# Optimization experiments

Hardware: AMD Instinct MI355X
Metric: run time of the kernel (lower is better)

## Reference

```python
import jax, jax.numpy as jnp
import numpy as np

VOCAB = 4194304
EMBED = 128
BATCH = 16384
NUM_DENSE = 13
NUM_CAT = 26
BOT_DIMS = (512, 256, 128)
TOP_DIMS = (1024, 1024, 512, 256, 1)


def _dense_params(key, fan_in, fan_out):
    kw, kb = jax.random.split(key)
    w = jax.random.normal(kw, (fan_in, fan_out), jnp.float32) * np.sqrt(2.0 / (fan_in + fan_out))
    b = jax.random.normal(kb, (fan_out,), jnp.float32) * np.sqrt(1.0 / fan_out)
    return w, b


def setup_inputs() -> dict:
    key = jax.random.key(0)
    ks = jax.random.split(key, 16)
    inp = {}
    inp['x_dense'] = jax.random.normal(ks[0], (BATCH, NUM_DENSE), jnp.float32)
    inp['x_cat'] = jax.random.randint(ks[1], (BATCH, NUM_CAT), 0, VOCAB, dtype=jnp.int32)
    # embedding table: uniform(0,1) * 1/sqrt(vocab)
    inp['embedding_table'] = jax.random.uniform(ks[2], (VOCAB, EMBED), jnp.float32) * np.float32(1.0 / np.sqrt(VOCAB))
    # bottom MLP params
    fan_in = NUM_DENSE
    for i, d in enumerate(BOT_DIMS):
        w, b = _dense_params(ks[3 + i], fan_in, d)
        inp[f'w_bot{i}'], inp[f'b_bot{i}'] = w, b
        fan_in = d
    # top MLP params; input dim = embed_dim + n_triu(27) = 128 + 378 = 506
    n_feat = 1 + NUM_CAT  # 27
    fan_in = EMBED + n_feat * (n_feat + 1) // 2
    for i, d in enumerate(TOP_DIMS):
        w, b = _dense_params(ks[8 + i], fan_in, d)
        inp[f'w_top{i}'], inp[f'b_top{i}'] = w, b
        fan_in = d
    return inp


def _forward(x_dense, x_cat, embedding_table,
             w_bot0, b_bot0, w_bot1, b_bot1, w_bot2, b_bot2,
             w_top0, b_top0, w_top1, b_top1, w_top2, b_top2,
             w_top3, b_top3, w_top4, b_top4):
    B = x_dense.shape[0]
    # bottom MLP
    h = x_dense
    for w, b in ((w_bot0, b_bot0), (w_bot1, b_bot1), (w_bot2, b_bot2)):
        h = jax.nn.relu(h @ w + b)
    bot_out = h  # [B, 128]
    feat = bot_out.reshape(B, -1, EMBED)  # [B, 1, 128]
    # embedding gather (irregular access)
    idx = (x_cat.reshape(-1) % VOCAB)
    emb = embedding_table[idx].reshape(B, NUM_CAT, EMBED)  # [B, 26, 128]
    stack = jnp.concatenate([feat, emb], axis=1)  # [B, 27, 128]
    # self interaction + upper-triangular (incl. diagonal) extraction
    xact = jnp.einsum('bnd,bmd->bnm', stack, stack)  # [B, 27, 27]
    i, j = jnp.triu_indices(stack.shape[1])
    inter = xact[:, i, j]  # [B, 378]
    top = jnp.concatenate([bot_out, inter], axis=-1)  # [B, 506]
    tops = ((w_top0, b_top0), (w_top1, b_top1), (w_top2, b_top2), (w_top3, b_top3), (w_top4, b_top4))
    for li, (w, b) in enumerate(tops):
        top = top @ w + b
        if li < len(tops) - 1:
            top = jax.nn.relu(top)
    return top  # [B, 1] logits


def reference(x_dense, x_cat, embedding_table,
              w_bot0, b_bot0, w_bot1, b_bot1, w_bot2, b_bot2,
              w_top0, b_top0, w_top1, b_top1, w_top2, b_top2,
              w_top3, b_top3, w_top4, b_top4):
    return _forward(x_dense, x_cat, embedding_table,
                    w_bot0, b_bot0, w_bot1, b_bot1, w_bot2, b_bot2,
                    w_top0, b_top0, w_top1, b_top1, w_top2, b_top2,
                    w_top3, b_top3, w_top4, b_top4)
```

## Files before the change

### kernel.cpp

```cpp
#include <hip/hip_runtime.h>
#include <cstdint>
#include <cstddef>

#define BATCH 16384
#define VOCAB_MASK (4194304 - 1)

typedef __attribute__((ext_vector_type(4))) float f32x4;
typedef __attribute__((ext_vector_type(8))) __bf16 bf16x8;

static_assert(sizeof(bf16x8) == 16, "bf16x8 must be 16 bytes");

static __device__ __forceinline__ __bf16 f2bf(float f) {
  union { float f; unsigned u; } in; in.f = f;
  unsigned r = in.u + 0x7FFF + ((in.u >> 16) & 1);
  union { unsigned short s; __bf16 b; } out; out.s = (unsigned short)(r >> 16);
  return out.b;
}
static __device__ __forceinline__ float bf2f(__bf16 b) {
  union { __bf16 b; unsigned short s; } in; in.b = b;
  union { unsigned u; float f; } out; out.u = ((unsigned)in.s) << 16;
  return out.f;
}

#define GLDS16(g, l) __builtin_amdgcn_global_load_lds( \
    (const __attribute__((address_space(1))) unsigned int*)(g), \
    (__attribute__((address_space(3))) unsigned int*)(l), 16, 0, 0)

static __device__ __forceinline__ unsigned swz16(unsigned b) {
  return b ^ ((((b >> 6) & 3u) ^ ((b >> 8) & 3u)) << 4);
}
static __device__ __forceinline__ bf16x8 lds_frag(const char* smem, unsigned base,
                                                  unsigned r, unsigned cg) {
  unsigned b = r * 64u + cg;
  return *(const bf16x8*)(smem + base + swz16(b));
}

struct TJob { const float* W; __bf16* WT; int K, N, Kp, tx, off; };
struct TJobs { TJob j[7]; };

__global__ __launch_bounds__(256) void transpose_all(TJobs js, int njobs)
{
  __shared__ float tile[64][65];
  int b = blockIdx.x;
  int ji = 0;
  #pragma unroll
  for (int i = 1; i < 7; ++i) if (i < njobs && b >= js.j[i].off) ji = i;
  const TJob jb = js.j[ji];
  int lb = b - jb.off;
  int bx = lb % jb.tx, by = lb / jb.tx;
  const int kb = bx * 64, nb = by * 64;
  const int tx = threadIdx.x & 63, ty = threadIdx.x >> 6;
  #pragma unroll
  for (int i = 0; i < 64; i += 4) {
    int k = kb + ty + i, n = nb + tx;
    tile[ty + i][tx] = (k < jb.K && n < jb.N) ? jb.W[(size_t)k * jb.N + n] : 0.f;
  }
  __syncthreads();
  #pragma unroll
  for (int i = 0; i < 64; i += 4) {
    int n = nb + ty + i, k = kb + tx;
    if (n < jb.N && k < jb.Kp) jb.WT[(size_t)n * jb.Kp + k] = f2bf(tile[tx][ty + i]);
  }
}

__global__ __launch_bounds__(256) void bottom_fused(
    const float* __restrict__ x,
    const __bf16* __restrict__ w0t, const float* __restrict__ b0,
    const __bf16* __restrict__ w1t, const float* __restrict__ b1,
    const __bf16* __restrict__ w2t, const float* __restrict__ b2,
    __bf16* __restrict__ h2out)
{
  __shared__ __bf16 h0s[32][520];
  __shared__ __bf16 h1s[32][264];
  __shared__ __bf16 As[32][40];
  __shared__ __bf16 Bs[256][32];
  const int tid = threadIdx.x, lane = tid & 63, w = tid >> 6;
  const int r0 = blockIdx.x * 32;
  const int srow_b = lane >> 2;
  const int scol_b = (lane & 3) * 8;
  const unsigned rA = lane & 15, cgw = (lane >> 4) * 8;

  for (int idx = tid; idx < 32 * 40; idx += 256) {
    int row = idx / 40, k = idx - row * 40;
    float v = (k < 13) ? x[(size_t)(r0 + row) * 13 + k] : 0.f;
    As[row][k] = f2bf(v);
  }

  #pragma unroll
  for (int p = 0; p < 2; ++p) {
    __syncthreads();
    #pragma unroll
    for (int c = 0; c < 4; ++c) {
      int row = w * 64 + c * 16 + srow_b;
      GLDS16(w0t + (size_t)(p * 256 + row) * 32 + scol_b, &Bs[row][scol_b]);
    }
    __syncthreads();
    bf16x8 a[2], bv[4];
    #pragma unroll
    for (int m = 0; m < 2; ++m) a[m] = *(const bf16x8*)&As[rA + m * 16][cgw];
    #pragma unroll
    for (int n = 0; n < 4; ++n) bv[n] = *(const bf16x8*)&Bs[w * 64 + n * 16 + rA][cgw];
    f32x4 acc[2][4] = {};
    #pragma unroll
    for (int m = 0; m < 2; ++m)
      #pragma unroll
      for (int n = 0; n < 4; ++n)
        acc[m][n] = __builtin_amdgcn_mfma_f32_16x16x32_bf16(a[m], bv[n], acc[m][n], 0, 0, 0);
    #pragma unroll
    for (int m = 0; m < 2; ++m)
      #pragma unroll
      for (int n = 0; n < 4; ++n) {
        int col = p * 256 + w * 64 + n * 16 + (int)rA;
        float bb = b0[col];
        #pragma unroll
        for (int r = 0; r < 4; ++r) {
          int row = m * 16 + (lane >> 4) * 4 + r;
          h0s[row][col] = f2bf(fmaxf(acc[m][n][r] + bb, 0.f));
        }
      }
  }

  f32x4 acc1[2][4] = {};
  for (int k0 = 0; k0 < 512; k0 += 32) {
    __syncthreads();
    #pragma unroll
    for (int c = 0; c < 4; ++c) {
      int row = w * 64 + c * 16 + srow_b;
      GLDS16(w1t + (size_t)row * 512 + k0 + scol_b, &Bs[row][scol_b]);
    }
    __syncthreads();
    bf16x8 a[2], bv[4];
    #pragma unroll
    for (int m = 0; m < 2; ++m) a[m] = *(const bf16x8*)&h0s[rA + m * 16][k0 + cgw];
    #pragma unroll
    for (int n = 0; n < 4; ++n) bv[n] = *(const bf16x8*)&Bs[w * 64 + n * 16 + rA][cgw];
    #pragma unroll
    for (int m = 0; m < 2; ++m)
      #pragma unroll
      for (int n = 0; n < 4; ++n)
        acc1[m][n] = __builtin_amdgcn_mfma_f32_16x16x32_bf16(a[m], bv[n], acc1[m][n], 0, 0, 0);
  }
  #pragma unroll
  for (int m = 0; m < 2; ++m)
    #pragma unroll
    for (int n = 0; n < 4; ++n) {
      int col = w * 64 + n * 16 + (int)rA;
      float bb = b1[col];
      #pragma unroll
      for (int r = 0; r < 4; ++r) {
        int row = m * 16 + (lane >> 4) * 4 + r;
        h1s[row][col] = f2bf(fmaxf(acc1[m][n][r] + bb, 0.f));
      }
    }

  f32x4 acc2[2][2] = {};
  for (int k0 = 0; k0 < 256; k0 += 32) {
    __syncthreads();
    #pragma unroll
    for (int c = 0; c < 2; ++c) {
      int row = w * 32 + c * 16 + srow_b;
      GLDS16(w2t + (size_t)row * 256 + k0 + scol_b, &Bs[row][scol_b]);
    }
    __syncthreads();
    bf16x8 a[2], bv[2];
    #pragma unroll
    for (int m = 0; m < 2; ++m) a[m] = *(const bf16x8*)&h1s[rA + m * 16][k0 + cgw];
    #pragma unroll
    for (int n = 0; n < 2; ++n) bv[n] = *(const bf16x8*)&Bs[w * 32 + n * 16 + rA][cgw];
    #pragma unroll
    for (int m = 0; m < 2; ++m)
      #pragma unroll
      for (int n = 0; n < 2; ++n)
        acc2[m][n] = __builtin_amdgcn_mfma_f32_16x16x32_bf16(a[m], bv[n], acc2[m][n], 0, 0, 0);
  }
  #pragma unroll
  for (int m = 0; m < 2; ++m)
    #pragma unroll
    for (int n = 0; n < 2; ++n) {
      int col = w * 32 + n * 16 + (int)rA;
      float bb = b2[col];
      #pragma unroll
      for (int r = 0; r < 4; ++r) {
        int row = m * 16 + (lane >> 4) * 4 + r;
        h2out[(size_t)(r0 + row) * 128 + col] = f2bf(fmaxf(acc2[m][n][r] + bb, 0.f));
      }
    }
}

__global__ __launch_bounds__(512, 2) void gemm_8ph(
    const __bf16* __restrict__ A, const __bf16* __restrict__ WT,
    const float* __restrict__ bias, __bf16* __restrict__ C,
    int N, int sA, int K, int gm)
{
  __shared__ __align__(16) char smem[65536];
  const int tid = threadIdx.x, lane = tid & 63, w = tid >> 6;
  const int wm = w >> 2, wn = w & 3;

  int nb = gridDim.x;
  int id = blockIdx.x;
  int swz = ((nb & 7) == 0) ? ((id & 7) * (nb >> 3) + (id >> 3)) : id;
  const int m0 = (swz % gm) * 256, n0 = (swz / gm) * 256;

  unsigned Ld[2]; const __bf16* sAp[2]; const __bf16* sBp[2];
  #pragma unroll
  for (int h = 0; h < 2; ++h) {
    unsigned L = h * 8192u + (unsigned)w * 1024u + (unsigned)lane * 16u;
    unsigned Ls = swz16(L);
    Ld[h] = L;
    int srow = Ls >> 6, scb = Ls & 63;
    sAp[h] = A  + (size_t)(m0 + srow) * sA + (scb >> 1);
    sBp[h] = WT + (size_t)(n0 + srow) * K  + (scb >> 1);
  }

  #define STAGE_A(kt, p) { GLDS16(sAp[0] + (kt)*32, smem + (p)*32768 + Ld[0]); \
                           GLDS16(sAp[1] + (kt)*32, smem + (p)*32768 + Ld[1]); }
  #define STAGE_B(kt, p) { GLDS16(sBp[0] + (kt)*32, smem + (p)*32768 + 16384 + Ld[0]); \
                           GLDS16(sBp[1] + (kt)*32, smem + (p)*32768 + 16384 + Ld[1]); }

  const unsigned cg = (lane >> 4) * 16u;
  const unsigned rA = (lane & 15);

  f32x4 acc[8][4] = {};
  const int iters = (K >> 5) >> 1;

  STAGE_B(0, 0); STAGE_A(0, 0); STAGE_B(1, 1);
  asm volatile("s_waitcnt vmcnt(2)" ::: "memory");
  __builtin_amdgcn_s_barrier();
  __builtin_amdgcn_sched_barrier(0);

  for (int i = 0; i < iters; ++i) {
    const int t = 2 * i;
    const bool more = (i + 1 < iters);

    bf16x8 a0[4], b0[4];
    #pragma unroll
    for (int m = 0; m < 4; ++m) a0[m] = lds_frag(smem, 0, wm * 128 + m * 16 + rA, cg);
    #pragma unroll
    for (int n = 0; n < 4; ++n) b0[n] = lds_frag(smem, 16384, wn * 64 + n * 16 + rA, cg);
    STAGE_A(t + 1, 1);
    __builtin_amdgcn_s_barrier();
    asm volatile("s_waitcnt lgkmcnt(0)" ::: "memory");
    __builtin_amdgcn_sched_barrier(0);
    __builtin_amdgcn_s_setprio(1);
    #pragma unroll
    for (int m = 0; m < 4; ++m)
      #pragma unroll
      for (int n = 0; n < 4; ++n)
        acc[m][n] = __builtin_amdgcn_mfma_f32_16x16x32_bf16(a0[m], b0[n], acc[m][n], 0, 0, 0);
    __builtin_amdgcn_s_setprio(0);
    __builtin_amdgcn_s_barrier();
    __builtin_amdgcn_sched_barrier(0);

    bf16x8 a1[4];
    #pragma unroll
    for (int m = 0; m < 4; ++m) a1[m] = lds_frag(smem, 0, wm * 128 + 64 + m * 16 + rA, cg);
    if (more) STAGE_B(t + 2, 0);
    __builtin_amdgcn_s_barrier();
    asm volatile("s_waitcnt lgkmcnt(0)" ::: "memory");
    __builtin_amdgcn_sched_barrier(0);
    __builtin_amdgcn_s_setprio(1);
    #pragma unroll
    for (int m = 0; m < 4; ++m)
      #pragma unroll
      for (int n = 0; n < 4; ++n)
        acc[4 + m][n] = __builtin_amdgcn_mfma_f32_16x16x32_bf16(a1[m], b0[n], acc[4 + m][n], 0, 0, 0);
    __builtin_amdgcn_s_setprio(0);
    if (more) { asm volatile("s_waitcnt vmcnt(2)" ::: "memory"); }
    else      { asm volatile("s_waitcnt vmcnt(0)" ::: "memory"); }
    __builtin_amdgcn_s_barrier();
    __builtin_amdgcn_sched_barrier(0);

    bf16x8 a2[4], b2[4];
    #pragma unroll
    for (int m = 0; m < 4; ++m) a2[m] = lds_frag(smem, 32768, wm * 128 + m * 16 + rA, cg);
    #pragma unroll
    for (int n = 0; n < 4; ++n) b2[n] = lds_frag(smem, 32768 + 16384, wn * 64 + n * 16 + rA, cg);
    if (more) STAGE_A(t + 2, 0);
    __builtin_amdgcn_s_barrier();
    asm volatile("s_waitcnt lgkmcnt(0)" ::: "memory");
    __builtin_amdgcn_sched_barrier(0);
    __builtin_amdgcn_s_setprio(1);
    #pragma unroll
    for (int m = 0; m < 4; ++m)
      #pragma unroll
      for (int n = 0; n < 4; ++n)
        acc[m][n] = __builtin_amdgcn_mfma_f32_16x16x32_bf16(a2[m], b2[n], acc[m][n], 0, 0, 0);
    __builtin_amdgcn_s_setprio(0);
    __builtin_amdgcn_s_barrier();
    __builtin_amdgcn_sched_barrier(0);

    bf16x8 a3[4];
    #pragma unroll
    for (int m = 0; m < 4; ++m) a3[m] = lds_frag(smem, 32768, wm * 128 + 64 + m * 16 + rA, cg);
    if (more) STAGE_B(t + 3, 1);
    __builtin_amdgcn_s_barrier();
    asm volatile("s_waitcnt lgkmcnt(0)" ::: "memory");
    __builtin_amdgcn_sched_barrier(0);
    __builtin_amdgcn_s_setprio(1);
    #pragma unroll
    for (int m = 0; m < 4; ++m)
      #pragma unroll
      for (int n = 0; n < 4; ++n)
        acc[4 + m][n] = __builtin_amdgcn_mfma_f32_16x16x32_bf16(a3[m], b2[n], acc[4 + m][n], 0, 0, 0);
    __builtin_amdgcn_s_setprio(0);
    if (more) { asm volatile("s_waitcnt vmcnt(2)" ::: "memory"); }
    __builtin_amdgcn_s_barrier();
    __builtin_amdgcn_sched_barrier(0);
  }

  #pragma unroll
  for (int n = 0; n < 4; ++n) {
    int col = n0 + wn * 64 + n * 16 + (lane & 15);
    float bv = bias[col];
    #pragma unroll
    for (int m = 0; m < 8; ++m) {
      #pragma unroll
      for (int r = 0; r < 4; ++r) {
        int row = m0 + wm * 128 + m * 16 + (lane >> 4) * 4 + r;
        float v = fmaxf(acc[m][n][r] + bv, 0.f);
        C[(size_t)row * N + col] = f2bf(v);
      }
    }
  }
  #undef STAGE_A
  #undef STAGE_B
}

__global__ __launch_bounds__(512, 2) void gemm_8ph_n128(
    const __bf16* __restrict__ A, const __bf16* __restrict__ WT,
    const float* __restrict__ bias, __bf16* __restrict__ C,
    int N, int sA, int K, int gm)
{
  __shared__ __align__(16) char smem[49152];
  const int tid = threadIdx.x, lane = tid & 63, w = tid >> 6;
  const int wm = w >> 1, wn = w & 1;

  int nb = gridDim.x;
  int id = blockIdx.x;
  int swz = ((nb & 7) == 0) ? ((id & 7) * (nb >> 3) + (id >> 3)) : id;
  const int m0 = (swz % gm) * 256, n0 = (swz / gm) * 128;

  unsigned Ld[2]; const __bf16* sAp[2]; const __bf16* sBp0;
  #pragma unroll
  for (int h = 0; h < 2; ++h) {
    unsigned L = h * 8192u + (unsigned)w * 1024u + (unsigned)lane * 16u;
    unsigned Ls = swz16(L);
    Ld[h] = L;
    int srow = Ls >> 6, scb = Ls & 63;
    sAp[h] = A + (size_t)(m0 + srow) * sA + (scb >> 1);
  }
  {
    unsigned L = (unsigned)w * 1024u + (unsigned)lane * 16u;
    unsigned Ls = swz16(L);
    int srow = Ls >> 6, scb = Ls & 63;
    sBp0 = WT + (size_t)(n0 + srow) * K + (scb >> 1);
  }

  #define STAGE_A2(kt, p) { GLDS16(sAp[0] + (kt)*32, smem + (p)*24576 + Ld[0]); \
                            GLDS16(sAp[1] + (kt)*32, smem + (p)*24576 + Ld[1]); }
  #define STAGE_B1(kt, p) { GLDS16(sBp0 + (kt)*32, smem + (p)*24576 + 16384 + Ld[0]); }

  const unsigned cg = (lane >> 4) * 16u;
  const unsigned rA = (lane & 15);

  f32x4 acc[4][4] = {};
  const int iters = (K >> 5) >> 1;

  STAGE_B1(0, 0); STAGE_A2(0, 0); STAGE_B1(1, 1);
  asm volatile("s_waitcnt vmcnt(1)" ::: "memory");
  __builtin_amdgcn_s_barrier();
  __builtin_amdgcn_sched_barrier(0);

  for (int i = 0; i < iters; ++i) {
    const int t = 2 * i;
    const bool more = (i + 1 < iters);

    bf16x8 a0[2], b0[4];
    #pragma unroll
    for (int m = 0; m < 2; ++m) a0[m] = lds_frag(smem, 0, wm * 64 + m * 16 + rA, cg);
    #pragma unroll
    for (int n = 0; n < 4; ++n) b0[n] = lds_frag(smem, 16384, wn * 64 + n * 16 + rA, cg);
    STAGE_A2(t + 1, 1);
    __builtin_amdgcn_s_barrier();
    asm volatile("s_waitcnt lgkmcnt(0)" ::: "memory");
    __builtin_amdgcn_sched_barrier(0);
    __builtin_amdgcn_s_setprio(1);
    #pragma unroll
    for (int m = 0; m < 2; ++m)
      #pragma unroll
      for (int n = 0; n < 4; ++n)
        acc[m][n] = __builtin_amdgcn_mfma_f32_16x16x32_bf16(a0[m], b0[n], acc[m][n], 0, 0, 0);
    __builtin_amdgcn_s_setprio(0);
    __builtin_amdgcn_s_barrier();
    __builtin_amdgcn_sched_barrier(0);

    bf16x8 a1[2];
    #pragma unroll
    for (int m = 0; m < 2; ++m) a1[m] = lds_frag(smem, 0, wm * 64 + 32 + m * 16 + rA, cg);
    if (more) STAGE_B1(t + 2, 0);
    __builtin_amdgcn_s_barrier();
    asm volatile("s_waitcnt lgkmcnt(0)" ::: "memory");
    __builtin_amdgcn_sched_barrier(0);
    __builtin_amdgcn_s_setprio(1);
    #pragma unroll
    for (int m = 0; m < 2; ++m)
      #pragma unroll
      for (int n = 0; n < 4; ++n)
        acc[2 + m][n] = __builtin_amdgcn_mfma_f32_16x16x32_bf16(a1[m], b0[n], acc[2 + m][n], 0, 0, 0);
    __builtin_amdgcn_s_setprio(0);
    if (more) { asm volatile("s_waitcnt vmcnt(1)" ::: "memory"); }
    else      { asm volatile("s_waitcnt vmcnt(0)" ::: "memory"); }
    __builtin_amdgcn_s_barrier();
    __builtin_amdgcn_sched_barrier(0);

    bf16x8 a2[2], b2[4];
    #pragma unroll
    for (int m = 0; m < 2; ++m) a2[m] = lds_frag(smem, 24576, wm * 64 + m * 16 + rA, cg);
    #pragma unroll
    for (int n = 0; n < 4; ++n) b2[n] = lds_frag(smem, 24576 + 16384, wn * 64 + n * 16 + rA, cg);
    if (more) STAGE_A2(t + 2, 0);
    __builtin_amdgcn_s_barrier();
    asm volatile("s_waitcnt lgkmcnt(0)" ::: "memory");
    __builtin_amdgcn_sched_barrier(0);
    __builtin_amdgcn_s_setprio(1);
    #pragma unroll
    for (int m = 0; m < 2; ++m)
      #pragma unroll
      for (int n = 0; n < 4; ++n)
        acc[m][n] = __builtin_amdgcn_mfma_f32_16x16x32_bf16(a2[m], b2[n], acc[m][n], 0, 0, 0);
    __builtin_amdgcn_s_setprio(0);
    __builtin_amdgcn_s_barrier();
    __builtin_amdgcn_sched_barrier(0);

    bf16x8 a3[2];
    #pragma unroll
    for (int m = 0; m < 2; ++m) a3[m] = lds_frag(smem, 24576, wm * 64 + 32 + m * 16 + rA, cg);
    if (more) STAGE_B1(t + 3, 1);
    __builtin_amdgcn_s_barrier();
    asm volatile("s_waitcnt lgkmcnt(0)" ::: "memory");
    __builtin_amdgcn_sched_barrier(0);
    __builtin_amdgcn_s_setprio(1);
    #pragma unroll
    for (int m = 0; m < 2; ++m)
      #pragma unroll
      for (int n = 0; n < 4; ++n)
        acc[2 + m][n] = __builtin_amdgcn_mfma_f32_16x16x32_bf16(a3[m], b2[n], acc[2 + m][n], 0, 0, 0);
    __builtin_amdgcn_s_setprio(0);
    if (more) { asm volatile("s_waitcnt vmcnt(1)" ::: "memory"); }
    __builtin_amdgcn_s_barrier();
    __builtin_amdgcn_sched_barrier(0);
  }

  #pragma unroll
  for (int n = 0; n < 4; ++n) {
    int col = n0 + wn * 64 + n * 16 + (lane & 15);
    float bv = bias[col];
    #pragma unroll
    for (int m = 0; m < 4; ++m) {
      #pragma unroll
      for (int r = 0; r < 4; ++r) {
        int row = m0 + wm * 64 + m * 16 + (lane >> 4) * 4 + r;
        float v = fmaxf(acc[m][n][r] + bv, 0.f);
        C[(size_t)row * N + col] = f2bf(v);
      }
    }
  }
  #undef STAGE_A2
  #undef STAGE_B1
}

__global__ __launch_bounds__(256) void gemm_glds(
    const __bf16* __restrict__ A, const __bf16* __restrict__ WT,
    const float* __restrict__ bias, __bf16* __restrict__ C,
    int N, int sA, int Kp)
{
  __shared__ __bf16 As[128][32];
  __shared__ __bf16 Bs[128][32];
  const int tid  = threadIdx.x;
  const int lane = tid & 63;
  const int wid  = tid >> 6;
  const int wr = wid >> 1, wc = wid & 1;
  const int m0 = blockIdx.x * 128, n0 = blockIdx.y * 128;

  const int srow = wid * 16 + (lane >> 2);
  const int scol = (lane & 3) * 8;
  const __bf16* Ag0 = A  + (size_t)(m0 + srow)      * sA + scol;
  const __bf16* Ag1 = A  + (size_t)(m0 + srow + 64) * sA + scol;
  const __bf16* Bg0 = WT + (size_t)(n0 + srow)      * Kp + scol;
  const __bf16* Bg1 = WT + (size_t)(n0 + srow + 64) * Kp + scol;
  __bf16* lA0 = &As[srow][scol];
  __bf16* lA1 = &As[srow + 64][scol];
  __bf16* lB0 = &Bs[srow][scol];
  __bf16* lB1 = &Bs[srow + 64][scol];

  f32x4 acc[4][4] = {};

  for (int k0 = 0; k0 < Kp; k0 += 32) {
    __syncthreads();
    GLDS16(Ag0 + k0, lA0);
    GLDS16(Ag1 + k0, lA1);
    GLDS16(Bg0 + k0, lB0);
    GLDS16(Bg1 + k0, lB1);
    __syncthreads();

    bf16x8 af[4], bfv[4];
    #pragma unroll
    for (int m = 0; m < 4; ++m)
      af[m] = *(const bf16x8*)&As[wr * 64 + m * 16 + (lane & 15)][(lane >> 4) * 8];
    #pragma unroll
    for (int n = 0; n < 4; ++n)
      bfv[n] = *(const bf16x8*)&Bs[wc * 64 + n * 16 + (lane & 15)][(lane >> 4) * 8];
    #pragma unroll
    for (int m = 0; m < 4; ++m)
      #pragma unroll
      for (int n = 0; n < 4; ++n)
        acc[m][n] = __builtin_amdgcn_mfma_f32_16x16x32_bf16(af[m], bfv[n], acc[m][n], 0, 0, 0);
  }

  #pragma unroll
  for (int m = 0; m < 4; ++m)
    #pragma unroll
    for (int n = 0; n < 4; ++n) {
      int col = n0 + wc * 64 + n * 16 + (lane & 15);
      float bv = bias[col];
      #pragma unroll
      for (int r = 0; r < 4; ++r) {
        int row = m0 + wr * 64 + m * 16 + (lane >> 4) * 4 + r;
        float v = fmaxf(acc[m][n][r] + bv, 0.f);
        C[(size_t)row * N + col] = f2bf(v);
      }
    }
}

__global__ __launch_bounds__(256) void interact_mfma(
    const __bf16* __restrict__ bot, const int* __restrict__ xcat,
    const float* __restrict__ emb, __bf16* __restrict__ top_in)
{
  __shared__ __bf16 st[4][32][136];
  const int tid = threadIdx.x, lane = tid & 63, w = tid >> 6;
  const int s = blockIdx.x * 4 + w;

  {
    const __bf16* bp = bot + (size_t)s * 128 + lane * 2;
    st[w][0][lane * 2]     = bp[0];
    st[w][0][lane * 2 + 1] = bp[1];
  }
  const int* xr = xcat + (size_t)s * 26;
  #pragma unroll
  for (int r = 1; r < 27; ++r) {
    int ridx = xr[r - 1] & VOCAB_MASK;
    float2 v = *(const float2*)(emb + (size_t)ridx * 128 + lane * 2);
    st[w][r][lane * 2]     = f2bf(v.x);
    st[w][r][lane * 2 + 1] = f2bf(v.y);
  }
  #pragma unroll
  for (int r = 27; r < 32; ++r) {
    st[w][r][lane * 2]     = f2bf(0.f);
    st[w][r][lane * 2 + 1] = f2bf(0.f);
  }

  f32x4 a00 = {}, a01 = {}, a11 = {};
  #pragma unroll
  for (int k0 = 0; k0 < 4; ++k0) {
    bf16x8 fr0 = *(const bf16x8*)&st[w][(lane & 15)][k0 * 32 + (lane >> 4) * 8];
    bf16x8 fr1 = *(const bf16x8*)&st[w][16 + (lane & 15)][k0 * 32 + (lane >> 4) * 8];
    a00 = __builtin_amdgcn_mfma_f32_16x16x32_bf16(fr0, fr0, a00, 0, 0, 0);
    a01 = __builtin_amdgcn_mfma_f32_16x16x32_bf16(fr0, fr1, a01, 0, 0, 0);
    a11 = __builtin_amdgcn_mfma_f32_16x16x32_bf16(fr1, fr1, a11, 0, 0, 0);
  }

  __bf16* op = top_in + (size_t)s * 512;
  op[lane * 2]     = st[w][0][lane * 2];
  op[lane * 2 + 1] = st[w][0][lane * 2 + 1];
  if (lane < 6) op[506 + lane] = f2bf(0.f);

  const int jc = lane & 15, rb = (lane >> 4) * 4;
  #pragma unroll
  for (int r = 0; r < 4; ++r) {
    {
      int i = rb + r, j = jc;
      if (i <= j) op[128 + i * 27 - i * (i - 1) / 2 + (j - i)] = f2bf(a00[r]);
    }
    {
      int i = rb + r, j = 16 + jc;
      if (j <= 26) op[128 + i * 27 - i * (i - 1) / 2 + (j - i)] = f2bf(a01[r]);
    }
    {
      int i = 16 + rb + r, j = 16 + jc;
      if (i <= j && j <= 26) op[128 + i * 27 - i * (i - 1) / 2 + (j - i)] = f2bf(a11[r]);
    }
  }
}

__global__ __launch_bounds__(256) void final_kernel(
    const __bf16* __restrict__ t3, const float* __restrict__ w4,
    const float* __restrict__ b4, float* __restrict__ out)
{
  int row  = blockIdx.x * 4 + (threadIdx.x >> 6);
  int lane = threadIdx.x & 63;
  const __bf16* tr = &t3[(size_t)row * 256 + lane * 4];
  float acc = 0.f;
  #pragma unroll
  for (int j = 0; j < 4; ++j) acc += bf2f(tr[j]) * w4[lane * 4 + j];
  #pragma unroll
  for (int off = 32; off; off >>= 1) acc += __shfl_down(acc, off);
  if (lane == 0) out[row] = acc + b4[0];
}

extern "C" void kernel_launch(void* const* d_in, const int* in_sizes, int n_in,
                              void* d_out, int out_size, void* d_ws, size_t ws_size,
                              hipStream_t stream)
{
  const float* x_dense = (const float*)d_in[0];
  const int*   x_cat   = (const int*)d_in[1];
  const float* emb     = (const float*)d_in[2];
  const float* wb[3] = {(const float*)d_in[3], (const float*)d_in[5], (const float*)d_in[7]};
  const float* bb[3] = {(const float*)d_in[4], (const float*)d_in[6], (const float*)d_in[8]};
  const float* wt[5] = {(const float*)d_in[9],  (const float*)d_in[11], (const float*)d_in[13],
                        (const float*)d_in[15], (const float*)d_in[17]};
  const float* bt[5] = {(const float*)d_in[10], (const float*)d_in[12], (const float*)d_in[14],
                        (const float*)d_in[16], (const float*)d_in[18]};
  float* out = (float*)d_out;

  char* ws = (char*)d_ws;
  const size_t MB = 1ull << 20;
  __bf16* wt_b0 = (__bf16*)(ws + 0 * MB);
  __bf16* wt_b1 = (__bf16*)(ws + 1 * MB);
  __bf16* wt_b2 = (__bf16*)(ws + 2 * MB);
  __bf16* wt_t0 = (__bf16*)(ws + 3 * MB);
  __bf16* wt_t1 = (__bf16*)(ws + 4 * MB);
  __bf16* wt_t2 = (__bf16*)(ws + 6 * MB);
  __bf16* wt_t3 = (__bf16*)(ws + 7 * MB);
  __bf16* h2     = (__bf16*)(ws + 8 * MB);
  __bf16* top_in = (__bf16*)(ws + 12 * MB);
  __bf16* t2     = (__bf16*)(ws + 12 * MB);
  __bf16* t1     = (__bf16*)(ws + 28 * MB);
  __bf16* t3     = (__bf16*)(ws + 28 * MB);
  __bf16* t0     = (__bf16*)(ws + 60 * MB);

  TJobs js;
  const float* Ws[7] = {wb[0], wb[1], wb[2], wt[0], wt[1], wt[2], wt[3]};
  __bf16* WTs[7] = {wt_b0, wt_b1, wt_b2, wt_t0, wt_t1, wt_t2, wt_t3};
  int Ks[7]  = {13, 512, 256, 506, 1024, 1024, 512};
  int Ns[7]  = {512, 256, 128, 1024, 1024, 512, 256};
  int Kps[7] = {32, 512, 256, 512, 1024, 1024, 512};
  int off = 0;
  for (int i = 0; i < 7; ++i) {
    int tx = (Kps[i] + 63) / 64, ty = (Ns[i] + 63) / 64;
    js.j[i] = TJob{Ws[i], WTs[i], Ks[i], Ns[i], Kps[i], tx, off};
    off += tx * ty;
  }
  transpose_all<<<dim3(off), dim3(256), 0, stream>>>(js, 7);

  bottom_fused<<<dim3(BATCH / 32), dim3(256), 0, stream>>>(
      x_dense, wt_b0, bb[0], wt_b1, bb[1], wt_b2, bb[2], h2);

  interact_mfma<<<dim3(BATCH / 4), dim3(256), 0, stream>>>(h2, x_cat, emb, top_in);

  gemm_8ph<<<dim3(256), dim3(512), 0, stream>>>(top_in, wt_t0, bt[0], t0, 1024, 512, 512, 64);
  gemm_8ph<<<dim3(256), dim3(512), 0, stream>>>(t0, wt_t1, bt[1], t1, 1024, 1024, 1024, 64);
  gemm_8ph_n128<<<dim3(256), dim3(512), 0, stream>>>(t1, wt_t2, bt[2], t2, 512, 1024, 1024, 64);
  gemm_glds<<<dim3(128, 2), dim3(256), 0, stream>>>(t2, wt_t3, bt[3], t3, 256, 512, 512);

  final_kernel<<<dim3(BATCH / 4), dim3(256), 0, stream>>>(t3, wt[4], bt[4], out);
}
```

Baseline: 198.8 us.

## Fuse bottom MLP with embedding interaction, and last top layer with final dot

```diff
diff --git a/kernel.cpp b/kernel.cpp
--- a/kernel.cpp
+++ b/kernel.cpp
@@ -7,6 +7,7 @@
 
 typedef __attribute__((ext_vector_type(4))) float f32x4;
 typedef __attribute__((ext_vector_type(8))) __bf16 bf16x8;
+typedef __attribute__((ext_vector_type(4))) __bf16 bf16x4;
 
 static_assert(sizeof(bf16x8) == 16, "bf16x8 must be 16 bytes");
 
@@ -63,27 +64,43 @@
   }
 }
 
-__global__ __launch_bounds__(256) void bottom_fused(
-    const float* __restrict__ x,
+__global__ __launch_bounds__(256) void bottom_interact(
+    const float* __restrict__ x, const int* __restrict__ xcat,
+    const float* __restrict__ emb,
     const __bf16* __restrict__ w0t, const float* __restrict__ b0,
     const __bf16* __restrict__ w1t, const float* __restrict__ b1,
     const __bf16* __restrict__ w2t, const float* __restrict__ b2,
-    __bf16* __restrict__ h2out)
+    __bf16* __restrict__ top_in)
 {
-  __shared__ __bf16 h0s[32][520];
-  __shared__ __bf16 h1s[32][264];
-  __shared__ __bf16 As[32][40];
-  __shared__ __bf16 Bs[256][32];
+  __shared__ __align__(16) char smem[77824];
   const int tid = threadIdx.x, lane = tid & 63, w = tid >> 6;
   const int r0 = blockIdx.x * 32;
   const int srow_b = lane >> 2;
   const int scol_b = (lane & 3) * 8;
   const unsigned rA = lane & 15, cgw = (lane >> 4) * 8;
 
+  #define AS_B(r,c) (smem + 8704  + (r)*80   + (c)*2)
+  #define BS_B(r,c) (smem + 11264 + (r)*64   + (c)*2)
+  #define H1_B(r,c) (smem + 27648 + (r)*528  + (c)*2)
+  #define H0_B(r,c) (smem + 44544 + (r)*1040 + (c)*2)
+  #define H2_B(r,c) (smem +         (r)*272  + (c)*2)
+
+  auto ld_gather = [&](float4 (&buf)[13], int s) {
+    const int* xs = xcat + (size_t)(r0 + w * 8 + s) * 26;
+    #pragma unroll
+    for (int i = 0; i < 13; ++i) {
+      int fi = 2 * i + (lane >> 5);
+      int ridx = xs[fi] & VOCAB_MASK;
+      buf[i] = *(const float4*)(emb + (size_t)ridx * 128 + (lane & 31) * 4);
+    }
+  };
+  float4 bufA[13], bufB[13];
+  ld_gather(bufA, 0);
+
   for (int idx = tid; idx < 32 * 40; idx += 256) {
     int row = idx / 40, k = idx - row * 40;
     float v = (k < 13) ? x[(size_t)(r0 + row) * 13 + k] : 0.f;
-    As[row][k] = f2bf(v);
+    *(__bf16*)AS_B(row, k) = f2bf(v);
   }
 
   #pragma unroll
@@ -92,14 +109,14 @@
     #pragma unroll
     for (int c = 0; c < 4; ++c) {
       int row = w * 64 + c * 16 + srow_b;
-      GLDS16(w0t + (size_t)(p * 256 + row) * 32 + scol_b, &Bs[row][scol_b]);
+      GLDS16(w0t + (size_t)(p * 256 + row) * 32 + scol_b, BS_B(row, scol_b));
     }
     __syncthreads();
     bf16x8 a[2], bv[4];
     #pragma unroll
-    for (int m = 0; m < 2; ++m) a[m] = *(const bf16x8*)&As[rA + m * 16][cgw];
-    #pragma unroll
-    for (int n = 0; n < 4; ++n) bv[n] = *(const bf16x8*)&Bs[w * 64 + n * 16 + rA][cgw];
+    for (int m = 0; m < 2; ++m) a[m] = *(const bf16x8*)AS_B(rA + m * 16, cgw);
+    #pragma unroll
+    for (int n = 0; n < 4; ++n) bv[n] = *(const bf16x8*)BS_B(w * 64 + n * 16 + rA, cgw);
     f32x4 acc[2][4] = {};
     #pragma unroll
     for (int m = 0; m < 2; ++m)
@@ -115,7 +132,7 @@
         #pragma unroll
         for (int r = 0; r < 4; ++r) {
           int row = m * 16 + (lane >> 4) * 4 + r;
-          h0s[row][col] = f2bf(fmaxf(acc[m][n][r] + bb, 0.f));
+          *(__bf16*)H0_B(row, col) = f2bf(fmaxf(acc[m][n][r] + bb, 0.f));
         }
       }
   }
@@ -126,14 +143,14 @@
     #pragma unroll
     for (int c = 0; c < 4; ++c) {
       int row = w * 64 + c * 16 + srow_b;
-      GLDS16(w1t + (size_t)row * 512 + k0 + scol_b, &Bs[row][scol_b]);
+      GLDS16(w1t + (size_t)row * 512 + k0 + scol_b, BS_B(row, scol_b));
     }
     __syncthreads();
     bf16x8 a[2], bv[4];
     #pragma unroll
-    for (int m = 0; m < 2; ++m) a[m] = *(const bf16x8*)&h0s[rA + m * 16][k0 + cgw];
-    #pragma unroll
-    for (int n = 0; n < 4; ++n) bv[n] = *(const bf16x8*)&Bs[w * 64 + n * 16 + rA][cgw];
+    for (int m = 0; m < 2; ++m) a[m] = *(const bf16x8*)H0_B(rA + m * 16, k0 + cgw);
+    #pragma unroll
+    for (int n = 0; n < 4; ++n) bv[n] = *(const bf16x8*)BS_B(w * 64 + n * 16 + rA, cgw);
     #pragma unroll
     for (int m = 0; m < 2; ++m)
       #pragma unroll
@@ -149,7 +166,7 @@
       #pragma unroll
       for (int r = 0; r < 4; ++r) {
         int row = m * 16 + (lane >> 4) * 4 + r;
-        h1s[row][col] = f2bf(fmaxf(acc1[m][n][r] + bb, 0.f));
+        *(__bf16*)H1_B(row, col) = f2bf(fmaxf(acc1[m][n][r] + bb, 0.f));
       }
     }
 
@@ -159,14 +176,14 @@
     #pragma unroll
     for (int c = 0; c < 2; ++c) {
       int row = w * 32 + c * 16 + srow_b;
-      GLDS16(w2t + (size_t)row * 256 + k0 + scol_b, &Bs[row][scol_b]);
+      GLDS16(w2t + (size_t)row * 256 + k0 + scol_b, BS_B(row, scol_b));
     }
     __syncthreads();
     bf16x8 a[2], bv[2];
     #pragma unroll
-    for (int m = 0; m < 2; ++m) a[m] = *(const bf16x8*)&h1s[rA + m * 16][k0 + cgw];
-    #pragma unroll
-    for (int n = 0; n < 2; ++n) bv[n] = *(const bf16x8*)&Bs[w * 32 + n * 16 + rA][cgw];
+    for (int m = 0; m < 2; ++m) a[m] = *(const bf16x8*)H1_B(rA + m * 16, k0 + cgw);
+    #pragma unroll
+    for (int n = 0; n < 2; ++n) bv[n] = *(const bf16x8*)BS_B(w * 32 + n * 16 + rA, cgw);
     #pragma unroll
     for (int m = 0; m < 2; ++m)
       #pragma unroll
@@ -182,9 +199,73 @@
       #pragma unroll
       for (int r = 0; r < 4; ++r) {
         int row = m * 16 + (lane >> 4) * 4 + r;
-        h2out[(size_t)(r0 + row) * 128 + col] = f2bf(fmaxf(acc2[m][n][r] + bb, 0.f));
-      }
-    }
+        *(__bf16*)H2_B(row, col) = f2bf(fmaxf(acc2[m][n][r] + bb, 0.f));
+      }
+    }
+
+  __syncthreads();
+
+  char* st_w = smem + 8704 + (unsigned)w * 8704u;
+  #pragma unroll
+  for (int r = 27; r < 32; ++r) *(unsigned*)(st_w + r * 272 + lane * 4) = 0;
+
+  #pragma unroll
+  for (int s = 0; s < 8; ++s) {
+    float4 (&cur)[13] = (s & 1) ? bufB : bufA;
+    float4 (&nxt)[13] = (s & 1) ? bufA : bufB;
+    const int sg = r0 + w * 8 + s;
+    __bf16* op = top_in + (size_t)sg * 512;
+
+    unsigned hv = *(const unsigned*)(smem + (unsigned)(w * 8 + s) * 272u + lane * 4);
+    *(unsigned*)(st_w + lane * 4) = hv;
+    ((unsigned*)op)[lane] = hv;
+    if (lane < 3) ((unsigned*)op)[253 + lane] = 0;
+
+    #pragma unroll
+    for (int i = 0; i < 13; ++i) {
+      int row = 1 + 2 * i + (lane >> 5);
+      float4 v = cur[i];
+      bf16x4 bv;
+      bv[0] = f2bf(v.x); bv[1] = f2bf(v.y); bv[2] = f2bf(v.z); bv[3] = f2bf(v.w);
+      *(bf16x4*)(st_w + row * 272 + (lane & 31) * 8) = bv;
+    }
+    if (s < 7) ld_gather(nxt, s + 1);
+
+    asm volatile("s_waitcnt lgkmcnt(0)" ::: "memory");
+    __builtin_amdgcn_sched_barrier(0);
+
+    f32x4 a00 = {}, a01 = {}, a11 = {};
+    #pragma unroll
+    for (int k0 = 0; k0 < 4; ++k0) {
+      bf16x8 fr0 = *(const bf16x8*)(st_w + (lane & 15) * 272 + k0 * 64 + (lane >> 4) * 16);
+      bf16x8 fr1 = *(const bf16x8*)(st_w + (16 + (lane & 15)) * 272 + k0 * 64 + (lane >> 4) * 16);
+      a00 = __builtin_amdgcn_mfma_f32_16x16x32_bf16(fr0, fr0, a00, 0, 0, 0);
+      a01 = __builtin_amdgcn_mfma_f32_16x16x32_bf16(fr0, fr1, a01, 0, 0, 0);
+      a11 = __builtin_amdgcn_mfma_f32_16x16x32_bf16(fr1, fr1, a11, 0, 0, 0);
+    }
+
+    const int jc = lane & 15, rb = (lane >> 4) * 4;
+    #pragma unroll
+    for (int r = 0; r < 4; ++r) {
+      {
+        int i = rb + r, j = jc;
+        if (i <= j) op[128 + i * 27 - i * (i - 1) / 2 + (j - i)] = f2bf(a00[r]);
+      }
+      {
+        int i = rb + r, j = 16 + jc;
+        if (j <= 26) op[128 + i * 27 - i * (i - 1) / 2 + (j - i)] = f2bf(a01[r]);
+      }
+      {
+        int i = 16 + rb + r, j = 16 + jc;
+        if (i <= j && j <= 26) op[128 + i * 27 - i * (i - 1) / 2 + (j - i)] = f2bf(a11[r]);
+      }
+    }
+  }
+  #undef AS_B
+  #undef BS_B
+  #undef H1_B
+  #undef H0_B
+  #undef H2_B
 }
 
 __global__ __launch_bounds__(512, 2) void gemm_8ph(
@@ -469,142 +550,76 @@
   #undef STAGE_B1
 }
 
-__global__ __launch_bounds__(256) void gemm_glds(
+__global__ __launch_bounds__(256) void gemm_t3_final(
     const __bf16* __restrict__ A, const __bf16* __restrict__ WT,
-    const float* __restrict__ bias, __bf16* __restrict__ C,
-    int N, int sA, int Kp)
+    const float* __restrict__ b3, const float* __restrict__ w4,
+    const float* __restrict__ b4, float* __restrict__ out)
 {
   __shared__ __bf16 As[128][32];
-  __shared__ __bf16 Bs[128][32];
-  const int tid  = threadIdx.x;
-  const int lane = tid & 63;
-  const int wid  = tid >> 6;
-  const int wr = wid >> 1, wc = wid & 1;
-  const int m0 = blockIdx.x * 128, n0 = blockIdx.y * 128;
-
+  __shared__ __bf16 Bs[256][32];
+  __shared__ float red[128][4];
+  const int tid = threadIdx.x, lane = tid & 63, wid = tid >> 6;
+  const int m0 = blockIdx.x * 128;
   const int srow = wid * 16 + (lane >> 2);
   const int scol = (lane & 3) * 8;
-  const __bf16* Ag0 = A  + (size_t)(m0 + srow)      * sA + scol;
-  const __bf16* Ag1 = A  + (size_t)(m0 + srow + 64) * sA + scol;
-  const __bf16* Bg0 = WT + (size_t)(n0 + srow)      * Kp + scol;
-  const __bf16* Bg1 = WT + (size_t)(n0 + srow + 64) * Kp + scol;
-  __bf16* lA0 = &As[srow][scol];
-  __bf16* lA1 = &As[srow + 64][scol];
-  __bf16* lB0 = &Bs[srow][scol];
-  __bf16* lB1 = &Bs[srow + 64][scol];
-
-  f32x4 acc[4][4] = {};
-
-  for (int k0 = 0; k0 < Kp; k0 += 32) {
-    __syncthreads();
-    GLDS16(Ag0 + k0, lA0);
-    GLDS16(Ag1 + k0, lA1);
-    GLDS16(Bg0 + k0, lB0);
-    GLDS16(Bg1 + k0, lB1);
-    __syncthreads();
-
-    bf16x8 af[4], bfv[4];
-    #pragma unroll
-    for (int m = 0; m < 4; ++m)
-      af[m] = *(const bf16x8*)&As[wr * 64 + m * 16 + (lane & 15)][(lane >> 4) * 8];
+  const __bf16* Ag0 = A + (size_t)(m0 + srow) * 512 + scol;
+  const __bf16* Ag1 = A + (size_t)(m0 + srow + 64) * 512 + scol;
+
+  f32x4 acc[8][4] = {};
+
+  for (int k0 = 0; k0 < 512; k0 += 32) {
+    __syncthreads();
+    GLDS16(Ag0 + k0, &As[srow][scol]);
+    GLDS16(Ag1 + k0, &As[srow + 64][scol]);
+    #pragma unroll
+    for (int c = 0; c < 4; ++c) {
+      int br = wid * 64 + c * 16 + (lane >> 2);
+      GLDS16(WT + (size_t)br * 512 + k0 + scol, &Bs[br][scol]);
+    }
+    __syncthreads();
+
+    bf16x8 af[8], bfv[4];
+    #pragma unroll
+    for (int m = 0; m < 8; ++m)
+      af[m] = *(const bf16x8*)&As[m * 16 + (lane & 15)][(lane >> 4) * 8];
     #pragma unroll
     for (int n = 0; n < 4; ++n)
-      bfv[n] = *(const bf16x8*)&Bs[wc * 64 + n * 16 + (lane & 15)][(lane >> 4) * 8];
-    #pragma unroll
-    for (int m = 0; m < 4; ++m)
+      bfv[n] = *(const bf16x8*)&Bs[wid * 64 + n * 16 + (lane & 15)][(lane >> 4) * 8];
+    #pragma unroll
+    for (int m = 0; m < 8; ++m)
       #pragma unroll
       for (int n = 0; n < 4; ++n)
         acc[m][n] = __builtin_amdgcn_mfma_f32_16x16x32_bf16(af[m], bfv[n], acc[m][n], 0, 0, 0);
   }
 
-  #pragma unroll
-  for (int m = 0; m < 4; ++m)
-    #pragma unroll
-    for (int n = 0; n < 4; ++n) {
-      int col = n0 + wc * 64 + n * 16 + (lane & 15);
-      float bv = bias[col];
-      #pragma unroll
-      for (int r = 0; r < 4; ++r) {
-        int row = m0 + wr * 64 + m * 16 + (lane >> 4) * 4 + r;
-        float v = fmaxf(acc[m][n][r] + bv, 0.f);
-        C[(size_t)row * N + col] = f2bf(v);
-      }
-    }
-}
-
-__global__ __launch_bounds__(256) void interact_mfma(
-    const __bf16* __restrict__ bot, const int* __restrict__ xcat,
-    const float* __restrict__ emb, __bf16* __restrict__ top_in)
-{
-  __shared__ __bf16 st[4][32][136];
-  const int tid = threadIdx.x, lane = tid & 63, w = tid >> 6;
-  const int s = blockIdx.x * 4 + w;
-
-  {
-    const __bf16* bp = bot + (size_t)s * 128 + lane * 2;
-    st[w][0][lane * 2]     = bp[0];
-    st[w][0][lane * 2 + 1] = bp[1];
-  }
-  const int* xr = xcat + (size_t)s * 26;
-  #pragma unroll
-  for (int r = 1; r < 27; ++r) {
-    int ridx = xr[r - 1] & VOCAB_MASK;
-    float2 v = *(const float2*)(emb + (size_t)ridx * 128 + lane * 2);
-    st[w][r][lane * 2]     = f2bf(v.x);
-    st[w][r][lane * 2 + 1] = f2bf(v.y);
-  }
-  #pragma unroll
-  for (int r = 27; r < 32; ++r) {
-    st[w][r][lane * 2]     = f2bf(0.f);
-    st[w][r][lane * 2 + 1] = f2bf(0.f);
-  }
-
-  f32x4 a00 = {}, a01 = {}, a11 = {};
-  #pragma unroll
-  for (int k0 = 0; k0 < 4; ++k0) {
-    bf16x8 fr0 = *(const bf16x8*)&st[w][(lane & 15)][k0 * 32 + (lane >> 4) * 8];
-    bf16x8 fr1 = *(const bf16x8*)&st[w][16 + (lane & 15)][k0 * 32 + (lane >> 4) * 8];
-    a00 = __builtin_amdgcn_mfma_f32_16x16x32_bf16(fr0, fr0, a00, 0, 0, 0);
-    a01 = __builtin_amdgcn_mfma_f32_16x16x32_bf16(fr0, fr1, a01, 0, 0, 0);
-    a11 = __builtin_amdgcn_mfma_f32_16x16x32_bf16(fr1, fr1, a11, 0, 0, 0);
-  }
-
-  __bf16* op = top_in + (size_t)s * 512;
-  op[lane * 2]     = st[w][0][lane * 2];
-  op[lane * 2 + 1] = st[w][0][lane * 2 + 1];
-  if (lane < 6) op[506 + lane] = f2bf(0.f);
-
-  const int jc = lane & 15, rb = (lane >> 4) * 4;
-  #pragma unroll
-  for (int r = 0; r < 4; ++r) {
-    {
-      int i = rb + r, j = jc;
-      if (i <= j) op[128 + i * 27 - i * (i - 1) / 2 + (j - i)] = f2bf(a00[r]);
-    }
-    {
-      int i = rb + r, j = 16 + jc;
-      if (j <= 26) op[128 + i * 27 - i * (i - 1) / 2 + (j - i)] = f2bf(a01[r]);
-    }
-    {
-      int i = 16 + rb + r, j = 16 + jc;
-      if (i <= j && j <= 26) op[128 + i * 27 - i * (i - 1) / 2 + (j - i)] = f2bf(a11[r]);
-    }
-  }
-}
-
-__global__ __launch_bounds__(256) void final_kernel(
-    const __bf16* __restrict__ t3, const float* __restrict__ w4,
-    const float* __restrict__ b4, float* __restrict__ out)
-{
-  int row  = blockIdx.x * 4 + (threadIdx.x >> 6);
-  int lane = threadIdx.x & 63;
-  const __bf16* tr = &t3[(size_t)row * 256 + lane * 4];
-  float acc = 0.f;
-  #pragma unroll
-  for (int j = 0; j < 4; ++j) acc += bf2f(tr[j]) * w4[lane * 4 + j];
-  #pragma unroll
-  for (int off = 32; off; off >>= 1) acc += __shfl_down(acc, off);
-  if (lane == 0) out[row] = acc + b4[0];
+  float pd[8][4];
+  #pragma unroll
+  for (int m = 0; m < 8; ++m)
+    #pragma unroll
+    for (int r = 0; r < 4; ++r) pd[m][r] = 0.f;
+  #pragma unroll
+  for (int n = 0; n < 4; ++n) {
+    int col = wid * 64 + n * 16 + (lane & 15);
+    float bb = b3[col];
+    float wc = w4[col];
+    #pragma unroll
+    for (int m = 0; m < 8; ++m)
+      #pragma unroll
+      for (int r = 0; r < 4; ++r)
+        pd[m][r] += fmaxf(acc[m][n][r] + bb, 0.f) * wc;
+  }
+  #pragma unroll
+  for (int m = 0; m < 8; ++m)
+    #pragma unroll
+    for (int r = 0; r < 4; ++r) {
+      float s = pd[m][r];
+      s += __shfl_xor(s, 1); s += __shfl_xor(s, 2);
+      s += __shfl_xor(s, 4); s += __shfl_xor(s, 8);
+      if ((lane & 15) == 0) red[m * 16 + (lane >> 4) * 4 + r][wid] = s;
+    }
+  __syncthreads();
+  if (tid < 128)
+    out[m0 + tid] = red[tid][0] + red[tid][1] + red[tid][2] + red[tid][3] + b4[0];
 }
 
 extern "C" void kernel_launch(void* const* d_in, const int* in_sizes, int n_in,
@@ -631,11 +646,9 @@
   __bf16* wt_t1 = (__bf16*)(ws + 4 * MB);
   __bf16* wt_t2 = (__bf16*)(ws + 6 * MB);
   __bf16* wt_t3 = (__bf16*)(ws + 7 * MB);
-  __bf16* h2     = (__bf16*)(ws + 8 * MB);
   __bf16* top_in = (__bf16*)(ws + 12 * MB);
   __bf16* t2     = (__bf16*)(ws + 12 * MB);
   __bf16* t1     = (__bf16*)(ws + 28 * MB);
-  __bf16* t3     = (__bf16*)(ws + 28 * MB);
   __bf16* t0     = (__bf16*)(ws + 60 * MB);
 
   TJobs js;
@@ -652,15 +665,12 @@
   }
   transpose_all<<<dim3(off), dim3(256), 0, stream>>>(js, 7);
 
-  bottom_fused<<<dim3(BATCH / 32), dim3(256), 0, stream>>>(
-      x_dense, wt_b0, bb[0], wt_b1, bb[1], wt_b2, bb[2], h2);
-
-  interact_mfma<<<dim3(BATCH / 4), dim3(256), 0, stream>>>(h2, x_cat, emb, top_in);
+  bottom_interact<<<dim3(BATCH / 32), dim3(256), 0, stream>>>(
+      x_dense, x_cat, emb, wt_b0, bb[0], wt_b1, bb[1], wt_b2, bb[2], top_in);
 
   gemm_8ph<<<dim3(256), dim3(512), 0, stream>>>(top_in, wt_t0, bt[0], t0, 1024, 512, 512, 64);
   gemm_8ph<<<dim3(256), dim3(512), 0, stream>>>(t0, wt_t1, bt[1], t1, 1024, 1024, 1024, 64);
   gemm_8ph_n128<<<dim3(256), dim3(512), 0, stream>>>(t1, wt_t2, bt[2], t2, 512, 1024, 1024, 64);
-  gemm_glds<<<dim3(128, 2), dim3(256), 0, stream>>>(t2, wt_t3, bt[3], t3, 256, 512, 512);
-
-  final_kernel<<<dim3(BATCH / 4), dim3(256), 0, stream>>>(t3, wt[4], bt[4], out);
-}
+
+  gemm_t3_final<<<dim3(128), dim3(256), 0, stream>>>(t2, wt_t3, bt[3], wt[4], bt[4], out);
+}
```

New measurement: 197.4 us. Within noise of the previous version (-0.7%).
